# Performance work log

Hardware: AMD Instinct MI355X
Metric: run time of the kernel (lower is better)

Reference implementation:

```python
import jax, jax.numpy as jnp
import numpy as np

B, V, C, M, CM, D, OUT = 16, 16, 64, 32, 16, 128, 600
VOCAB = {"cond": 4000, "proc": 2000, "drug": 600, "lab_item": 700, "lab_value": 2000, "inj_item": 400, "inj_value": 2000}


def _gru(x, Wih, Whh, bih, bhh):
    """Batch-first torch-style GRU. x: [N,T,D] -> (outputs [N,T,D], h_T [N,D])."""
    Dh = Whh.shape[1]

    def step(h, xt):
        gi = xt @ Wih.T + bih
        gh = h @ Whh.T + bhh
        ir, iz, ig = jnp.split(gi, 3, axis=-1)
        hr, hz, hg = jnp.split(gh, 3, axis=-1)
        r = jax.nn.sigmoid(ir + hr)
        z = jax.nn.sigmoid(iz + hz)
        n = jnp.tanh(ig + r * hg)
        h = (1.0 - z) * n + z * h
        return h, h

    h0 = jnp.zeros((x.shape[0], Dh), x.dtype)
    hT, ys = jax.lax.scan(step, h0, jnp.swapaxes(x, 0, 1))
    return jnp.swapaxes(ys, 0, 1), hT


def _hetero_mp(feats, Wself, Wmsg):
    """Heterogeneous message passing over node types on the fully-connected
    monitor<->visit-feature bipartite pattern: each node type combines a self
    transform with a transformed mean of the other node types, then ReLU.
    feats: list of [N,D]; Wself/Wmsg: [T,D,D]."""
    stacked = jnp.stack(feats)  # [T,N,D]
    total = jnp.sum(stacked, axis=0)
    T = stacked.shape[0]
    outs = []
    for t in range(T):
        others = (total - stacked[t]) / (T - 1)
        outs.append(jax.nn.relu(stacked[t] @ Wself[t] + others @ Wmsg[t]))
    return outs


def _forward(codes_cond, codes_proc, codes_drug, codes_lab_item, codes_lab_value,
             codes_inj_item, codes_inj_value, weight, age,
             emb_cond, emb_proc, emb_drug, emb_lab_item, emb_lab_value,
             emb_inj_item, emb_inj_value,
             mgru_Wih, mgru_Whh, mgru_bih, mgru_bhh,
             vgru_Wih, vgru_Whh, vgru_bih, vgru_bhh,
             gnn_Wself, gnn_Wmsg,
             fc_weight_W, fc_weight_b, fc_age_W, fc_age_b,
             fc_patient_W, fc_patient_b):
    # ---- visit-event features: embedding lookup + sum-pool over codes ----
    vis = {}
    for k, codes, emb in (("cond", codes_cond, emb_cond),
                          ("proc", codes_proc, emb_proc),
                          ("drug", codes_drug, emb_drug)):
        vis[k] = jnp.sum(emb[codes], axis=2)  # [B,V,D]
    visit_keys = ("cond", "proc", "drug")

    # ---- monitor-event pairs: (item * value) embeddings, GNN, two-level GRU ----
    pairs = (
        (codes_lab_item, codes_lab_value, emb_lab_item, emb_lab_value, "lab_item", (0, 2, 3, 4)),
        (codes_inj_item, codes_inj_value, emb_inj_item, emb_inj_value, "inj_item", (1, 2, 3, 4)),
    )
    hid = {}
    for p, (ci, cv, ei, ev, ikey, gidx) in enumerate(pairs):
        mon = jnp.sum(ei[ci] * ev[cv], axis=3)  # [B,V,M,D]
        feats = [mon.reshape(-1, D)]  # monitor node type, [B*V*M, D]
        for k in visit_keys:  # visit features repeated across monitors
            feats.append(jnp.broadcast_to(vis[k][:, :, None, :], (B, V, M, D)).reshape(-1, D))
        outs = _hetero_mp(feats, gnn_Wself[p], gnn_Wmsg[p])
        for t, k in enumerate((ikey,) + visit_keys):
            g = gidx[t]
            # monitor-level GRU over the M monitors of each visit
            o, _ = _gru(outs[t].reshape(B * V, M, D), mgru_Wih[g], mgru_Whh[g], mgru_bih[g], mgru_bhh[g])
            last = o[:, -1, :].reshape(B, V, D)  # last monitor state per visit
            # visit-level GRU (source uses visit_gru[feature_key1] for all keys)
            _, h = _gru(last, vgru_Wih[p], vgru_Whh[p], vgru_bih[p], vgru_bhh[p])
            hid[k] = h if k not in hid else hid[k] + h

    # ---- weight / age scalar features ----
    for k, x, W, b, vi in (("weight", weight, fc_weight_W, fc_weight_b, 2),
                           ("age", age, fc_age_W, fc_age_b, 3)):
        mask = (x != 0.0)[..., None]  # [B,V,1]
        xe = (x[..., None] * W[:, 0] + b) * mask  # Linear(1->D) then zero-mask
        _, h = _gru(xe, vgru_Wih[vi], vgru_Whh[vi], vgru_bih[vi], vgru_bhh[vi])
        hid[k] = h

    # ---- concat in dict-insertion order, then ReLU + Linear head ----
    pe = jnp.concatenate([hid["lab_item"], hid["cond"], hid["proc"], hid["drug"],
                          hid["inj_item"], hid["weight"], hid["age"]], axis=-1)  # [B, 7D]
    return jax.nn.relu(pe) @ fc_patient_W.T + fc_patient_b  # [B, OUT]


def setup_inputs() -> dict:
    key = jax.random.key(0)
    ks = iter(jax.random.split(key, 64))

    def nrm(shape, s=0.1):
        return (jax.random.normal(next(ks), shape) * s).astype(jnp.float32)

    def emb_table(vsz):
        t = nrm((vsz, D), 1.0)
        return t.at[0].set(0.0)  # padding_idx=0 row is zero

    inp = {}
    inp["codes_cond"] = jax.random.randint(next(ks), (B, V, C), 0, VOCAB["cond"], dtype=jnp.int32)
    inp["codes_proc"] = jax.random.randint(next(ks), (B, V, C), 0, VOCAB["proc"], dtype=jnp.int32)
    inp["codes_drug"] = jax.random.randint(next(ks), (B, V, C), 0, VOCAB["drug"], dtype=jnp.int32)
    inp["codes_lab_item"] = jax.random.randint(next(ks), (B, V, M, CM), 0, VOCAB["lab_item"], dtype=jnp.int32)
    inp["codes_lab_value"] = jax.random.randint(next(ks), (B, V, M, CM), 0, VOCAB["lab_value"], dtype=jnp.int32)
    inp["codes_inj_item"] = jax.random.randint(next(ks), (B, V, M, CM), 0, VOCAB["inj_item"], dtype=jnp.int32)
    inp["codes_inj_value"] = jax.random.randint(next(ks), (B, V, M, CM), 0, VOCAB["inj_value"], dtype=jnp.int32)
    inp["weight"] = jax.random.uniform(next(ks), (B, V), minval=0.1, maxval=1.0, dtype=jnp.float32)
    inp["age"] = jax.random.uniform(next(ks), (B, V), minval=0.1, maxval=1.0, dtype=jnp.float32)
    inp["emb_cond"] = emb_table(VOCAB["cond"])
    inp["emb_proc"] = emb_table(VOCAB["proc"])
    inp["emb_drug"] = emb_table(VOCAB["drug"])
    inp["emb_lab_item"] = emb_table(VOCAB["lab_item"])
    inp["emb_lab_value"] = emb_table(VOCAB["lab_value"])
    inp["emb_inj_item"] = emb_table(VOCAB["inj_item"])
    inp["emb_inj_value"] = emb_table(VOCAB["inj_value"])
    inp["mgru_Wih"] = nrm((5, 3 * D, D))
    inp["mgru_Whh"] = nrm((5, 3 * D, D))
    inp["mgru_bih"] = nrm((5, 3 * D))
    inp["mgru_bhh"] = nrm((5, 3 * D))
    inp["vgru_Wih"] = nrm((4, 3 * D, D))
    inp["vgru_Whh"] = nrm((4, 3 * D, D))
    inp["vgru_bih"] = nrm((4, 3 * D))
    inp["vgru_bhh"] = nrm((4, 3 * D))
    inp["gnn_Wself"] = nrm((2, 4, D, D))
    inp["gnn_Wmsg"] = nrm((2, 4, D, D))
    inp["fc_weight_W"] = nrm((D, 1))
    inp["fc_weight_b"] = nrm((D,))
    inp["fc_age_W"] = nrm((D, 1))
    inp["fc_age_b"] = nrm((D,))
    inp["fc_patient_W"] = nrm((OUT, 7 * D))
    inp["fc_patient_b"] = nrm((OUT,))
    return inp


def reference(codes_cond, codes_proc, codes_drug, codes_lab_item, codes_lab_value,
              codes_inj_item, codes_inj_value, weight, age,
              emb_cond, emb_proc, emb_drug, emb_lab_item, emb_lab_value,
              emb_inj_item, emb_inj_value,
              mgru_Wih, mgru_Whh, mgru_bih, mgru_bhh,
              vgru_Wih, vgru_Whh, vgru_bih, vgru_bhh,
              gnn_Wself, gnn_Wmsg,
              fc_weight_W, fc_weight_b, fc_age_W, fc_age_b,
              fc_patient_W, fc_patient_b):
    return _forward(codes_cond, codes_proc, codes_drug, codes_lab_item, codes_lab_value,
                    codes_inj_item, codes_inj_value, weight, age,
                    emb_cond, emb_proc, emb_drug, emb_lab_item, emb_lab_value,
                    emb_inj_item, emb_inj_value,
                    mgru_Wih, mgru_Whh, mgru_bih, mgru_bhh,
                    vgru_Wih, vgru_Whh, vgru_bih, vgru_bhh,
                    gnn_Wself, gnn_Wmsg,
                    fc_weight_W, fc_weight_b, fc_age_W, fc_age_b,
                    fc_patient_W, fc_patient_b)
```

## Files before the change

kernel.cpp:

```cpp
#include <hip/hip_runtime.h>
#include <math.h>

#define B_   16
#define V_   16
#define C_   64
#define M_   32
#define CM_  16
#define D_   128
#define OUT_ 600
#define NSEQ 256
#define NROW 8192

typedef __attribute__((ext_vector_type(8))) short bf16x8;
typedef __attribute__((ext_vector_type(4))) short bf16x4;
typedef __attribute__((ext_vector_type(4))) float f32x4;

__device__ __forceinline__ unsigned short f2bf(float x) {
  union { float f; unsigned u; } v; v.f = x;
  unsigned r = v.u + 0x7fff + ((v.u >> 16) & 1);
  return (unsigned short)(r >> 16);
}
__device__ __forceinline__ float bf2f(short s) {
  union { unsigned u; float f; } v;
  v.u = ((unsigned)(unsigned short)s) << 16;
  return v.f;
}
__device__ __forceinline__ float fsig(float x)  { return __fdividef(1.f, 1.f + __expf(-x)); }
__device__ __forceinline__ float ftanh(float x) { return 1.f - 2.f*__fdividef(1.f, __expf(2.f*x) + 1.f); }

__device__ __forceinline__ void ldsbar() {
  asm volatile("s_waitcnt lgkmcnt(0)" ::: "memory");
  __builtin_amdgcn_s_barrier();
  asm volatile("" ::: "memory");
}

constexpr int OFF_VISB  = 98304;
constexpr int OFF_MONB  = 147456;
constexpr int OFF_W12T  = 2244608;
constexpr int OFF_WIHB  = 2375680;
constexpr int OFF_WIHTV = 2498560;
constexpr int OFF_XE    = 2695168;
constexpr int OFF_LAST  = 27926528;
constexpr int OFF_VH    = 29171712;

__global__ __launch_bounds__(256) void k_prepvis(
    const float* __restrict__ Wself, const float* __restrict__ Wmsg,
    const float* __restrict__ mWih,  const float* __restrict__ vWih,
    const float* __restrict__ wgt,   const float* __restrict__ age,
    const float* __restrict__ fwW,   const float* __restrict__ fwB,
    const float* __restrict__ faW,   const float* __restrict__ faB,
    const int* __restrict__ cc, const int* __restrict__ cp, const int* __restrict__ cd,
    const float* __restrict__ ec, const float* __restrict__ ep, const float* __restrict__ ed,
    const int* __restrict__ cli, const int* __restrict__ clv,
    const int* __restrict__ cii, const int* __restrict__ civ,
    const float* __restrict__ eli, const float* __restrict__ elv,
    const float* __restrict__ eii, const float* __restrict__ eiv,
    short* __restrict__ w12t, short* __restrict__ wihb,
    float* __restrict__ wihTv, float* __restrict__ xe,
    short* __restrict__ visb, short* __restrict__ monb)
{
  int bx = blockIdx.x, tid = threadIdx.x;
  if (bx < 1024) {
    int lin = bx*256 + tid;
    int pt = lin >> 15, rem = lin & 32767;
    int n = rem >> 8, k = rem & 255;
    float v;
    if (k < 128) v = Wself[pt*16384 + k*128 + n] - Wmsg[pt*16384 + k*128 + n]*(1.f/3.f);
    else         v = Wmsg[pt*16384 + (k-128)*128 + n]*(1.f/3.f);
    w12t[lin] = (short)f2bf(v);
  } else if (bx < 1984) {
    int lin = (bx-1024)*256 + tid;
    wihb[lin] = (short)f2bf(mWih[lin]);
  } else if (bx < 2752) {
    int lin = (bx-1984)*256 + tid;
    int g = lin / 49152, rem2 = lin % 49152;
    int k = rem2 / 384, j = rem2 % 384;
    wihTv[lin] = vWih[g*49152 + j*128 + k];
  } else if (bx < 3008) {
    int lin = (bx-2752)*256 + tid;
    int which = lin >> 15, rem2 = lin & 32767;
    int n = rem2 >> 7, d = rem2 & 127;
    float x  = which ? age[n] : wgt[n];
    float Wv = which ? faW[d] : fwW[d];
    float bb = which ? faB[d] : fwB[d];
    xe[lin] = (x != 0.0f) ? (x*Wv + bb) : 0.0f;
  } else if (bx < 3392) {
    int idx = (bx-3008)*256 + tid;
    int type = idx >> 15;
    int r = idx & 32767;
    int bv = r >> 7, d = r & 127;
    const int*   codes = (type==0) ? cc : (type==1) ? cp : cd;
    const float* emb   = (type==0) ? ec : (type==1) ? ep : ed;
    float acc = 0.f;
    for (int c = 0; c < C_; ++c) {
      int code = codes[bv*C_ + c];
      acc += emb[code*D_ + d];
    }
    visb[(type*NSEQ + bv)*D_ + d] = (short)f2bf(acc);
  } else {
    int rowid = (bx-3392)*2 + (tid >> 7);
    int p = rowid >> 13, bvm = rowid & 8191;
    int d = tid & 127;
    const int* ci = p ? cii : cli;  const int* cv = p ? civ : clv;
    const float* ei = p ? eii : eli; const float* ev = p ? eiv : elv;
    float acc = 0.f;
    #pragma unroll
    for (int c2 = 0; c2 < CM_; ++c2) {
      int iv = ci[bvm*CM_ + c2];
      int vv = cv[bvm*CM_ + c2];
      acc += ei[iv*D_ + d] * ev[vv*D_ + d];
    }
    monb[((size_t)p*NROW + bvm)*D_ + d] = (short)f2bf(acc);
  }
}

__global__ __launch_bounds__(512, 1) void k_ggru(
    const short* __restrict__ monb, const short* __restrict__ visb,
    const short* __restrict__ w12t, const short* __restrict__ wihb,
    const float* __restrict__ Wself, const float* __restrict__ mWhh,
    const float* __restrict__ mbih, const float* __restrict__ mbhh,
    float* __restrict__ last)
{
  const int run  = blockIdx.x >> 4;
  const int pair = blockIdx.x & 15;
  const int p = run >> 2, t = run & 3;
  const int g = (run % 4 == 0) ? (run / 4) : (run % 4 + 1);
  const int tid = threadIdx.x;
  const int w = tid >> 6;
  const int lane = tid & 63;
  const int c = lane & 15, q = lane >> 4;
  const int j = w*16 + c;

  __shared__ short hb[2][4][16][40];
  __shared__ __align__(16) short Ys[2][16][136];
  __shared__ __align__(16) short Xl[2][2048];

  for (int idx = tid; idx < 2*4*16*40; idx += 512)
    ((short*)hb)[idx] = 0;

  bf16x8 bW12[8];
  #pragma unroll
  for (int kt = 0; kt < 8; ++kt)
    bW12[kt] = *(const bf16x8*)(w12t + (size_t)run*32768 + (size_t)j*256 + kt*32 + q*8);

  bf16x8 bWs[4];
  if (t == 0) {
    const float* wsp = Wself + (size_t)run*16384 + j;
    #pragma unroll
    for (int kt = 0; kt < 4; ++kt) {
      bf16x8 tt;
      #pragma unroll
      for (int i = 0; i < 8; ++i)
        tt[i] = (short)f2bf(wsp[(kt*32 + q*8 + i)*128]);
      bWs[kt] = tt;
    }
  } else {
    #pragma unroll
    for (int kt = 0; kt < 4; ++kt) bWs[kt] = bW12[kt+4];
  }

  f32x4 Cpre = (f32x4){0.f,0.f,0.f,0.f};
  {
    const int bvc = pair*16 + c;
    #pragma unroll
    for (int kt = 0; kt < 4; ++kt) {
      const int ko = kt*32 + q*8;
      bf16x8 v0 = *(const bf16x8*)(visb + (size_t)(0*NSEQ + bvc)*128 + ko);
      bf16x8 v1 = *(const bf16x8*)(visb + (size_t)(1*NSEQ + bvc)*128 + ko);
      bf16x8 v2 = *(const bf16x8*)(visb + (size_t)(2*NSEQ + bvc)*128 + ko);
      bf16x8 vs;
      #pragma unroll
      for (int i = 0; i < 8; ++i)
        vs[i] = (short)f2bf(bf2f(v0[i]) + bf2f(v1[i]) + bf2f(v2[i]));
      Cpre = __builtin_amdgcn_mfma_f32_16x16x32_bf16(vs, bW12[kt+4], Cpre, 0, 0, 0);
    }
    if (t > 0) {
      #pragma unroll
      for (int kt = 0; kt < 4; ++kt) {
        const int ko = kt*32 + q*8;
        bf16x8 fv = *(const bf16x8*)(visb + (size_t)((t-1)*NSEQ + bvc)*128 + ko);
        Cpre = __builtin_amdgcn_mfma_f32_16x16x32_bf16(fv, bW12[kt], Cpre, 0, 0, 0);
      }
    }
  }

  bf16x8 bWih[3][4];
  #pragma unroll
  for (int gate = 0; gate < 3; ++gate)
    #pragma unroll
    for (int kt = 0; kt < 4; ++kt)
      bWih[gate][kt] = *(const bf16x8*)(wihb + ((size_t)g*384 + gate*128 + j)*128 + kt*32 + q*8);

  bf16x8 bWhh[3][4];
  #pragma unroll
  for (int gate = 0; gate < 3; ++gate) {
    const float* wp = mWhh + ((size_t)g*384 + gate*128 + j)*128 + q*8;
    #pragma unroll
    for (int kt = 0; kt < 4; ++kt) {
      float4 lo = *(const float4*)(wp + kt*32);
      float4 hi = *(const float4*)(wp + kt*32 + 4);
      bf16x8 tt;
      tt[0]=(short)f2bf(lo.x); tt[1]=(short)f2bf(lo.y); tt[2]=(short)f2bf(lo.z); tt[3]=(short)f2bf(lo.w);
      tt[4]=(short)f2bf(hi.x); tt[5]=(short)f2bf(hi.y); tt[6]=(short)f2bf(hi.z); tt[7]=(short)f2bf(hi.w);
      bWhh[gate][kt] = tt;
    }
  }
  const float bs0 = mbih[g*384 +       j] + mbhh[g*384 +       j];
  const float bs1 = mbih[g*384 + 128 + j] + mbhh[g*384 + 128 + j];
  const float bi2 = mbih[g*384 + 256 + j];
  const float bh2 = mbhh[g*384 + 256 + j];

  const bool stg = (tid < 256);
  const int xr_ = (tid >> 4) & 15, xu = tid & 15;
  const int bv = pair*16 + xr_;
  const short* fsrc = monb + ((size_t)p*NROW + (size_t)bv*32)*128 + xu*8;
  const int xdofs = xr_*128 + (((xu*16) ^ ((xr_&7)<<4)) >> 1);
  short* xdst0 = &Xl[0][xdofs];
  short* xdst1 = &Xl[1][xdofs];

  if (stg) {
    *(bf16x8*)xdst0 = *(const bf16x8*)fsrc;
    *(bf16x8*)xdst1 = *(const bf16x8*)(fsrc + 128);
  }
  float hf[4] = {0.f,0.f,0.f,0.f};
  const int ktw = w >> 1;
  const int kkw = (w & 1)*16 + c;
  ldsbar();

  {
    const char* xbase = (const char*)&Xl[0][0];
    f32x4 accY = Cpre;
    #pragma unroll
    for (int kt = 0; kt < 4; ++kt) {
      bf16x8 aX = *(const bf16x8*)(xbase + c*256 + ((kt*64 + q*16) ^ ((c&7)<<4)));
      accY = __builtin_amdgcn_mfma_f32_16x16x32_bf16(aX, bWs[kt], accY, 0, 0, 0);
    }
    #pragma unroll
    for (int reg = 0; reg < 4; ++reg)
      Ys[0][q*4 + reg][w*16 + c] = (short)f2bf(fmaxf(accY[reg], 0.f));
  }
  ldsbar();

  #pragma unroll 1
  for (int m = 0; m < 32; ++m) {
    const int cur = m & 1, nxt = cur ^ 1;

    bf16x8 xnext;
    if (stg && m < 30) xnext = *(const bf16x8*)(fsrc + (size_t)(m+2)*128);

    f32x4 accY = Cpre;
    if (m < 31) {
      const char* xbase = (const char*)&Xl[nxt][0];
      #pragma unroll
      for (int kt = 0; kt < 4; ++kt) {
        bf16x8 aX = *(const bf16x8*)(xbase + c*256 + ((kt*64 + q*16) ^ ((c&7)<<4)));
        accY = __builtin_amdgcn_mfma_f32_16x16x32_bf16(aX, bWs[kt], accY, 0, 0, 0);
      }
    }

    bf16x8 ah[4], a2[4];
    #pragma unroll
    for (int kt = 0; kt < 4; ++kt) {
      ah[kt] = *(const bf16x8*)&hb[cur][kt][c][q*8];
      a2[kt] = *(const bf16x8*)&Ys[cur][c][kt*32 + q*8];
    }
    f32x4 acc0 = (f32x4){0.f,0.f,0.f,0.f};
    f32x4 acc1 = (f32x4){0.f,0.f,0.f,0.f};
    f32x4 aG2  = (f32x4){0.f,0.f,0.f,0.f};
    f32x4 aH2  = (f32x4){0.f,0.f,0.f,0.f};
    #pragma unroll
    for (int kt = 0; kt < 4; ++kt) {
      acc0 = __builtin_amdgcn_mfma_f32_16x16x32_bf16(ah[kt], bWhh[0][kt], acc0, 0, 0, 0);
      acc1 = __builtin_amdgcn_mfma_f32_16x16x32_bf16(ah[kt], bWhh[1][kt], acc1, 0, 0, 0);
      aH2  = __builtin_amdgcn_mfma_f32_16x16x32_bf16(ah[kt], bWhh[2][kt], aH2,  0, 0, 0);
    }
    #pragma unroll
    for (int kt = 0; kt < 4; ++kt) {
      acc0 = __builtin_amdgcn_mfma_f32_16x16x32_bf16(a2[kt], bWih[0][kt], acc0, 0, 0, 0);
      acc1 = __builtin_amdgcn_mfma_f32_16x16x32_bf16(a2[kt], bWih[1][kt], acc1, 0, 0, 0);
      aG2  = __builtin_amdgcn_mfma_f32_16x16x32_bf16(a2[kt], bWih[2][kt], aG2,  0, 0, 0);
    }

    if (m < 31) {
      #pragma unroll
      for (int reg = 0; reg < 4; ++reg)
        Ys[nxt][q*4 + reg][w*16 + c] = (short)f2bf(fmaxf(accY[reg], 0.f));
    }
    if (stg && m < 30) *(bf16x8*)(cur ? xdst1 : xdst0) = xnext;

    #pragma unroll
    for (int reg = 0; reg < 4; ++reg) {
      float rr = fsig(acc0[reg] + bs0);
      float zz = fsig(acc1[reg] + bs1);
      float nn = ftanh(aG2[reg] + bi2 + rr*(aH2[reg] + bh2));
      float hnew = (1.f - zz)*nn + zz*hf[reg];
      hf[reg] = hnew;
      hb[nxt][ktw][q*4 + reg][kkw] = (short)f2bf(hnew);
    }
    ldsbar();
  }

  #pragma unroll
  for (int reg = 0; reg < 4; ++reg)
    last[((size_t)run*NSEQ + pair*16 + q*4 + reg)*D_ + j] = hf[reg];
}

__global__ __launch_bounds__(512, 1) void k_vgru(
    const float* __restrict__ last, const float* __restrict__ xe,
    const float* __restrict__ vWih, const float* __restrict__ vWhh,
    const float* __restrict__ vbih, const float* __restrict__ vbhh,
    float* __restrict__ vh)
{
  const int run = blockIdx.x;
  const int vidx = (run < 4) ? 0 : (run < 8) ? 1 : (run - 6);
  const int tid = threadIdx.x;
  const int w = tid >> 6;
  const int lane = tid & 63;
  const int c = lane & 15, q = lane >> 4;
  const int j = w*16 + c;

  __shared__ short hb[2][4][16][40];
  __shared__ __align__(16) short Xl[2][2048];

  for (int idx = tid; idx < 2*4*16*40; idx += 512)
    ((short*)hb)[idx] = 0;

  bf16x8 bWih[3][4], bWhh[3][4];
  #pragma unroll
  for (int gate = 0; gate < 3; ++gate) {
    const float* wi = vWih + ((size_t)vidx*384 + gate*128 + j)*128 + q*8;
    const float* wh = vWhh + ((size_t)vidx*384 + gate*128 + j)*128 + q*8;
    #pragma unroll
    for (int kt = 0; kt < 4; ++kt) {
      float4 a0 = *(const float4*)(wi + kt*32);
      float4 a1 = *(const float4*)(wi + kt*32 + 4);
      float4 b0 = *(const float4*)(wh + kt*32);
      float4 b1 = *(const float4*)(wh + kt*32 + 4);
      bf16x8 ti, th;
      ti[0]=(short)f2bf(a0.x); ti[1]=(short)f2bf(a0.y); ti[2]=(short)f2bf(a0.z); ti[3]=(short)f2bf(a0.w);
      ti[4]=(short)f2bf(a1.x); ti[5]=(short)f2bf(a1.y); ti[6]=(short)f2bf(a1.z); ti[7]=(short)f2bf(a1.w);
      th[0]=(short)f2bf(b0.x); th[1]=(short)f2bf(b0.y); th[2]=(short)f2bf(b0.z); th[3]=(short)f2bf(b0.w);
      th[4]=(short)f2bf(b1.x); th[5]=(short)f2bf(b1.y); th[6]=(short)f2bf(b1.z); th[7]=(short)f2bf(b1.w);
      bWih[gate][kt] = ti;
      bWhh[gate][kt] = th;
    }
  }
  const float bs0 = vbih[vidx*384 +       j] + vbhh[vidx*384 +       j];
  const float bs1 = vbih[vidx*384 + 128 + j] + vbhh[vidx*384 + 128 + j];
  const float bi2 = vbih[vidx*384 + 256 + j];
  const float bh2 = vbhh[vidx*384 + 256 + j];

  const bool stg = (tid < 256);
  const int xr_ = (tid >> 4) & 15, xu = tid & 15;
  const float* xsrc = ((run < 8) ? (last + ((size_t)run*NSEQ + xr_*16)*D_)
                                 : (xe + ((size_t)(run-8)*NSEQ + xr_*16)*D_)) + xu*8;
  const int xdofs = xr_*128 + (((xu*16) ^ ((xr_&7)<<4)) >> 1);
  short* xdst0 = &Xl[0][xdofs];
  short* xdst1 = &Xl[1][xdofs];

  auto stageX = [&](short* dst, int v) {
    const float* s = xsrc + (size_t)v*D_;
    float4 lo = *(const float4*)s;
    float4 hi = *(const float4*)(s + 4);
    bf16x8 t;
    t[0]=(short)f2bf(lo.x); t[1]=(short)f2bf(lo.y); t[2]=(short)f2bf(lo.z); t[3]=(short)f2bf(lo.w);
    t[4]=(short)f2bf(hi.x); t[5]=(short)f2bf(hi.y); t[6]=(short)f2bf(hi.z); t[7]=(short)f2bf(hi.w);
    *(bf16x8*)dst = t;
  };
  if (stg) { stageX(xdst0, 0); stageX(xdst1, 1); }

  float hf[4] = {0.f,0.f,0.f,0.f};
  const int ktw = w >> 1;
  const int kkw = (w & 1)*16 + c;
  ldsbar();

  f32x4 giA[3], giB[3];
  {
    const char* xbase = (const char*)&Xl[0][0];
    #pragma unroll
    for (int gate = 0; gate < 3; ++gate) giA[gate] = (f32x4){0.f,0.f,0.f,0.f};
    #pragma unroll
    for (int kt = 0; kt < 4; ++kt) {
      bf16x8 ax = *(const bf16x8*)(xbase + c*256 + ((kt*64 + q*16) ^ ((c&7)<<4)));
      giA[0] = __builtin_amdgcn_mfma_f32_16x16x32_bf16(ax, bWih[0][kt], giA[0], 0, 0, 0);
      giA[1] = __builtin_amdgcn_mfma_f32_16x16x32_bf16(ax, bWih[1][kt], giA[1], 0, 0, 0);
      giA[2] = __builtin_amdgcn_mfma_f32_16x16x32_bf16(ax, bWih[2][kt], giA[2], 0, 0, 0);
    }
  }
  ldsbar();

  auto step = [&](int v, f32x4 (&gcur)[3], f32x4 (&gnext)[3]) {
    const int cur = v & 1, nxt = cur ^ 1;
    if (v < 15) {
      const char* xbase = (const char*)&Xl[nxt][0];
      #pragma unroll
      for (int gate = 0; gate < 3; ++gate) gnext[gate] = (f32x4){0.f,0.f,0.f,0.f};
      #pragma unroll
      for (int kt = 0; kt < 4; ++kt) {
        bf16x8 ax = *(const bf16x8*)(xbase + c*256 + ((kt*64 + q*16) ^ ((c&7)<<4)));
        gnext[0] = __builtin_amdgcn_mfma_f32_16x16x32_bf16(ax, bWih[0][kt], gnext[0], 0, 0, 0);
        gnext[1] = __builtin_amdgcn_mfma_f32_16x16x32_bf16(ax, bWih[1][kt], gnext[1], 0, 0, 0);
        gnext[2] = __builtin_amdgcn_mfma_f32_16x16x32_bf16(ax, bWih[2][kt], gnext[2], 0, 0, 0);
      }
    }
    bf16x8 ah[4];
    #pragma unroll
    for (int kt = 0; kt < 4; ++kt)
      ah[kt] = *(const bf16x8*)&hb[cur][kt][c][q*8];
    f32x4 a0 = gcur[0], a1 = gcur[1];
    f32x4 aH2 = (f32x4){0.f,0.f,0.f,0.f};
    #pragma unroll
    for (int kt = 0; kt < 4; ++kt) {
      a0  = __builtin_amdgcn_mfma_f32_16x16x32_bf16(ah[kt], bWhh[0][kt], a0,  0, 0, 0);
      a1  = __builtin_amdgcn_mfma_f32_16x16x32_bf16(ah[kt], bWhh[1][kt], a1,  0, 0, 0);
      aH2 = __builtin_amdgcn_mfma_f32_16x16x32_bf16(ah[kt], bWhh[2][kt], aH2, 0, 0, 0);
    }
    if (stg && v < 14) stageX(cur ? xdst1 : xdst0, v + 2);
    #pragma unroll
    for (int reg = 0; reg < 4; ++reg) {
      float rr = fsig(a0[reg] + bs0);
      float zz = fsig(a1[reg] + bs1);
      float nn = ftanh(gcur[2][reg] + bi2 + rr*(aH2[reg] + bh2));
      float hnew = (1.f - zz)*nn + zz*hf[reg];
      hf[reg] = hnew;
      hb[nxt][ktw][q*4 + reg][kkw] = (short)f2bf(hnew);
    }
    ldsbar();
  };

  #pragma unroll 1
  for (int v2 = 0; v2 < 8; ++v2) {
    step(2*v2,     giA, giB);
    step(2*v2 + 1, giB, giA);
  }

  #pragma unroll
  for (int reg = 0; reg < 4; ++reg)
    vh[((size_t)run*16 + q*4 + reg)*D_ + j] = hf[reg];
}

__global__ __launch_bounds__(256) void k_head(
    const float* __restrict__ vh, const float* __restrict__ Wp,
    const float* __restrict__ bp, float* __restrict__ out)
{
  const int o = blockIdx.x;
  const int tid = threadIdx.x;
  const int b = tid & 15, kc = tid >> 4;
  const int a1[7] = {0,1,2,3,4,8,9};
  const int a2[7] = {-1,5,6,7,-1,-1,-1};
  const float4* wb = (const float4*)(Wp + (size_t)o*896 + kc*56);
  float acc = 0.f;
  #pragma unroll
  for (int i = 0; i < 14; ++i) {
// ... 53 lines not shown
  const float* Wself= (const float*)d_in[24];
  const float* Wmsg = (const float*)d_in[25];
  const float* fwW  = (const float*)d_in[26];
  const float* fwB  = (const float*)d_in[27];
  const float* faW  = (const float*)d_in[28];
  const float* faB  = (const float*)d_in[29];
  const float* Wp   = (const float*)d_in[30];
  const float* bp   = (const float*)d_in[31];
  float* out = (float*)d_out;
  float* ws  = (float*)d_ws;

  short* visb  = (short*)(ws + OFF_VISB);
  short* monb  = (short*)(ws + OFF_MONB);
  short* w12t  = (short*)(ws + OFF_W12T);
  short* wihb  = (short*)(ws + OFF_WIHB);
  float* wihTv = ws + OFF_WIHTV;
  float* xe    = ws + OFF_XE;
  float* last  = ws + OFF_LAST;
  float* vh    = ws + OFF_VH;

  k_prepvis<<<11584, 256, 0, stream>>>(Wself, Wmsg, mWih, vWih, wgt, age,
                                       fwW, fwB, faW, faB,
                                       cc, cp, cd, ec, ep, ed,
                                       cli, clv, cii, civ, eli, elv, eii, eiv,
                                       w12t, wihb, wihTv, xe, visb, monb);
  k_ggru<<<128, 512, 0, stream>>>(monb, visb, w12t, wihb, Wself,
                                  mWhh, mbih, mbhh, last);
  k_vgru<<<10, 512, 0, stream>>>(last, xe, vWih, vWhh, vbih, vbhh, vh);
  k_head<<<600, 256, 0, stream>>>(vh, Wp, bp, out);
}
```

Before: 245.9 us.

## Fuse visit GRU into monitor GRU kernel via last-block atomic counter handoff

Merges the separate visit-level GRU kernel into the monitor GRU kernel. Each of the 8 monitor runs uses an atomic counter so that the last of its 16 blocks goes on to run that run's visit GRU, and two extra blocks handle the weight/age sequences, which removes one kernel launch and its serialization gap. The visit GRU can start per run as soon as that run's monitor blocks finish, instead of waiting for all of them. It also drops the unused transposed vWih prep section from the prep kernel. The trade-off is threadfence/atomic overhead and a longer tail on the finishing blocks.

```diff
diff --git a/kernel.cpp b/kernel.cpp
--- a/kernel.cpp
+++ b/kernel.cpp
@@ -38,14 +38,14 @@
 constexpr int OFF_MONB  = 147456;
 constexpr int OFF_W12T  = 2244608;
 constexpr int OFF_WIHB  = 2375680;
-constexpr int OFF_WIHTV = 2498560;
+constexpr int OFF_CNT   = 2498560;
 constexpr int OFF_XE    = 2695168;
 constexpr int OFF_LAST  = 27926528;
 constexpr int OFF_VH    = 29171712;
 
 __global__ __launch_bounds__(256) void k_prepvis(
     const float* __restrict__ Wself, const float* __restrict__ Wmsg,
-    const float* __restrict__ mWih,  const float* __restrict__ vWih,
+    const float* __restrict__ mWih,
     const float* __restrict__ wgt,   const float* __restrict__ age,
     const float* __restrict__ fwW,   const float* __restrict__ fwB,
     const float* __restrict__ faW,   const float* __restrict__ faB,
@@ -56,11 +56,13 @@
     const float* __restrict__ eli, const float* __restrict__ elv,
     const float* __restrict__ eii, const float* __restrict__ eiv,
     short* __restrict__ w12t, short* __restrict__ wihb,
-    float* __restrict__ wihTv, float* __restrict__ xe,
-    short* __restrict__ visb, short* __restrict__ monb)
+    float* __restrict__ xe,
+    short* __restrict__ visb, short* __restrict__ monb,
+    int* __restrict__ cnt)
 {
   int bx = blockIdx.x, tid = threadIdx.x;
   if (bx < 1024) {
+    if (bx == 0 && tid < 16) cnt[tid] = 0;
     int lin = bx*256 + tid;
     int pt = lin >> 15, rem = lin & 32767;
     int n = rem >> 8, k = rem & 255;
@@ -71,21 +73,16 @@
   } else if (bx < 1984) {
     int lin = (bx-1024)*256 + tid;
     wihb[lin] = (short)f2bf(mWih[lin]);
-  } else if (bx < 2752) {
+  } else if (bx < 2240) {
     int lin = (bx-1984)*256 + tid;
-    int g = lin / 49152, rem2 = lin % 49152;
-    int k = rem2 / 384, j = rem2 % 384;
-    wihTv[lin] = vWih[g*49152 + j*128 + k];
-  } else if (bx < 3008) {
-    int lin = (bx-2752)*256 + tid;
     int which = lin >> 15, rem2 = lin & 32767;
     int n = rem2 >> 7, d = rem2 & 127;
     float x  = which ? age[n] : wgt[n];
     float Wv = which ? faW[d] : fwW[d];
     float bb = which ? faB[d] : fwB[d];
     xe[lin] = (x != 0.0f) ? (x*Wv + bb) : 0.0f;
-  } else if (bx < 3392) {
-    int idx = (bx-3008)*256 + tid;
+  } else if (bx < 2624) {
+    int idx = (bx-2240)*256 + tid;
     int type = idx >> 15;
     int r = idx & 32767;
     int bv = r >> 7, d = r & 127;
@@ -98,7 +95,7 @@
     }
     visb[(type*NSEQ + bv)*D_ + d] = (short)f2bf(acc);
   } else {
-    int rowid = (bx-3392)*2 + (tid >> 7);
+    int rowid = (bx-2624)*2 + (tid >> 7);
     int p = rowid >> 13, bvm = rowid & 8191;
     int d = tid & 127;
     const int* ci = p ? cii : cli;  const int* cv = p ? civ : clv;
@@ -119,12 +116,11 @@
     const short* __restrict__ w12t, const short* __restrict__ wihb,
     const float* __restrict__ Wself, const float* __restrict__ mWhh,
     const float* __restrict__ mbih, const float* __restrict__ mbhh,
-    float* __restrict__ last)
+    const float* __restrict__ vWih, const float* __restrict__ vWhh,
+    const float* __restrict__ vbih, const float* __restrict__ vbhh,
+    const float* __restrict__ xe, float* __restrict__ last,
+    float* __restrict__ vh, int* __restrict__ cnt)
 {
-  const int run  = blockIdx.x >> 4;
-  const int pair = blockIdx.x & 15;
-  const int p = run >> 2, t = run & 3;
-  const int g = (run % 4 == 0) ? (run / 4) : (run % 4 + 1);
   const int tid = threadIdx.x;
   const int w = tid >> 6;
   const int lane = tid & 63;
@@ -134,309 +130,316 @@
   __shared__ short hb[2][4][16][40];
   __shared__ __align__(16) short Ys[2][16][136];
   __shared__ __align__(16) short Xl[2][2048];
-
-  for (int idx = tid; idx < 2*4*16*40; idx += 512)
-    ((short*)hb)[idx] = 0;
-
-  bf16x8 bW12[8];
-  #pragma unroll
-  for (int kt = 0; kt < 8; ++kt)
-    bW12[kt] = *(const bf16x8*)(w12t + (size_t)run*32768 + (size_t)j*256 + kt*32 + q*8);
-
-  bf16x8 bWs[4];
-  if (t == 0) {
-    const float* wsp = Wself + (size_t)run*16384 + j;
-    #pragma unroll
-    for (int kt = 0; kt < 4; ++kt) {
-      bf16x8 tt;
-      #pragma unroll
-      for (int i = 0; i < 8; ++i)
-        tt[i] = (short)f2bf(wsp[(kt*32 + q*8 + i)*128]);
-      bWs[kt] = tt;
-    }
-  } else {
-    #pragma unroll
-    for (int kt = 0; kt < 4; ++kt) bWs[kt] = bW12[kt+4];
-  }
-
-  f32x4 Cpre = (f32x4){0.f,0.f,0.f,0.f};
-  {
-    const int bvc = pair*16 + c;
-    #pragma unroll
-    for (int kt = 0; kt < 4; ++kt) {
-      const int ko = kt*32 + q*8;
-      bf16x8 v0 = *(const bf16x8*)(visb + (size_t)(0*NSEQ + bvc)*128 + ko);
-      bf16x8 v1 = *(const bf16x8*)(visb + (size_t)(1*NSEQ + bvc)*128 + ko);
-      bf16x8 v2 = *(const bf16x8*)(visb + (size_t)(2*NSEQ + bvc)*128 + ko);
-      bf16x8 vs;
-      #pragma unroll
-      for (int i = 0; i < 8; ++i)
-        vs[i] = (short)f2bf(bf2f(v0[i]) + bf2f(v1[i]) + bf2f(v2[i]));
-      Cpre = __builtin_amdgcn_mfma_f32_16x16x32_bf16(vs, bW12[kt+4], Cpre, 0, 0, 0);
-    }
-    if (t > 0) {
+  __shared__ int dofin;
+
+  int vrun;
+
+  if (blockIdx.x < 128) {
+    const int run  = blockIdx.x >> 4;
+    const int pair = blockIdx.x & 15;
+    const int p = run >> 2, t = run & 3;
+    const int g = (run % 4 == 0) ? (run / 4) : (run % 4 + 1);
+
+    for (int idx = tid; idx < 2*4*16*40; idx += 512)
+      ((short*)hb)[idx] = 0;
+
+    bf16x8 bW12[8];
+    #pragma unroll
+    for (int kt = 0; kt < 8; ++kt)
+      bW12[kt] = *(const bf16x8*)(w12t + (size_t)run*32768 + (size_t)j*256 + kt*32 + q*8);
+
+    bf16x8 bWs[4];
+    if (t == 0) {
+      const float* wsp = Wself + (size_t)run*16384 + j;
+      #pragma unroll
+      for (int kt = 0; kt < 4; ++kt) {
+        bf16x8 tt;
+        #pragma unroll
+        for (int i = 0; i < 8; ++i)
+          tt[i] = (short)f2bf(wsp[(kt*32 + q*8 + i)*128]);
+        bWs[kt] = tt;
+      }
+    } else {
+      #pragma unroll
+      for (int kt = 0; kt < 4; ++kt) bWs[kt] = bW12[kt+4];
+    }
+
+    f32x4 Cpre = (f32x4){0.f,0.f,0.f,0.f};
+    {
+      const int bvc = pair*16 + c;
       #pragma unroll
       for (int kt = 0; kt < 4; ++kt) {
         const int ko = kt*32 + q*8;
-        bf16x8 fv = *(const bf16x8*)(visb + (size_t)((t-1)*NSEQ + bvc)*128 + ko);
-        Cpre = __builtin_amdgcn_mfma_f32_16x16x32_bf16(fv, bW12[kt], Cpre, 0, 0, 0);
-      }
-    }
-  }
-
-  bf16x8 bWih[3][4];
-  #pragma unroll
-  for (int gate = 0; gate < 3; ++gate)
-    #pragma unroll
-    for (int kt = 0; kt < 4; ++kt)
-      bWih[gate][kt] = *(const bf16x8*)(wihb + ((size_t)g*384 + gate*128 + j)*128 + kt*32 + q*8);
-
-  bf16x8 bWhh[3][4];
-  #pragma unroll
-  for (int gate = 0; gate < 3; ++gate) {
-    const float* wp = mWhh + ((size_t)g*384 + gate*128 + j)*128 + q*8;
-    #pragma unroll
-    for (int kt = 0; kt < 4; ++kt) {
-      float4 lo = *(const float4*)(wp + kt*32);
-      float4 hi = *(const float4*)(wp + kt*32 + 4);
-      bf16x8 tt;
-      tt[0]=(short)f2bf(lo.x); tt[1]=(short)f2bf(lo.y); tt[2]=(short)f2bf(lo.z); tt[3]=(short)f2bf(lo.w);
-      tt[4]=(short)f2bf(hi.x); tt[5]=(short)f2bf(hi.y); tt[6]=(short)f2bf(hi.z); tt[7]=(short)f2bf(hi.w);
-      bWhh[gate][kt] = tt;
-    }
-  }
-  const float bs0 = mbih[g*384 +       j] + mbhh[g*384 +       j];
-  const float bs1 = mbih[g*384 + 128 + j] + mbhh[g*384 + 128 + j];
-  const float bi2 = mbih[g*384 + 256 + j];
-  const float bh2 = mbhh[g*384 + 256 + j];
-
-  const bool stg = (tid < 256);
-  const int xr_ = (tid >> 4) & 15, xu = tid & 15;
-  const int bv = pair*16 + xr_;
-  const short* fsrc = monb + ((size_t)p*NROW + (size_t)bv*32)*128 + xu*8;
-  const int xdofs = xr_*128 + (((xu*16) ^ ((xr_&7)<<4)) >> 1);
-  short* xdst0 = &Xl[0][xdofs];
-  short* xdst1 = &Xl[1][xdofs];
-
-  if (stg) {
-    *(bf16x8*)xdst0 = *(const bf16x8*)fsrc;
-    *(bf16x8*)xdst1 = *(const bf16x8*)(fsrc + 128);
-  }
-  float hf[4] = {0.f,0.f,0.f,0.f};
-  const int ktw = w >> 1;
-  const int kkw = (w & 1)*16 + c;
-  ldsbar();
-
-  {
-    const char* xbase = (const char*)&Xl[0][0];
-    f32x4 accY = Cpre;
-    #pragma unroll
-    for (int kt = 0; kt < 4; ++kt) {
-      bf16x8 aX = *(const bf16x8*)(xbase + c*256 + ((kt*64 + q*16) ^ ((c&7)<<4)));
-      accY = __builtin_amdgcn_mfma_f32_16x16x32_bf16(aX, bWs[kt], accY, 0, 0, 0);
-    }
-    #pragma unroll
-    for (int reg = 0; reg < 4; ++reg)
-      Ys[0][q*4 + reg][w*16 + c] = (short)f2bf(fmaxf(accY[reg], 0.f));
-  }
-  ldsbar();
-
-  #pragma unroll 1
-  for (int m = 0; m < 32; ++m) {
-    const int cur = m & 1, nxt = cur ^ 1;
-
-    bf16x8 xnext;
-    if (stg && m < 30) xnext = *(const bf16x8*)(fsrc + (size_t)(m+2)*128);
-
-    f32x4 accY = Cpre;
-    if (m < 31) {
-      const char* xbase = (const char*)&Xl[nxt][0];
+        bf16x8 v0 = *(const bf16x8*)(visb + (size_t)(0*NSEQ + bvc)*128 + ko);
+        bf16x8 v1 = *(const bf16x8*)(visb + (size_t)(1*NSEQ + bvc)*128 + ko);
+        bf16x8 v2 = *(const bf16x8*)(visb + (size_t)(2*NSEQ + bvc)*128 + ko);
+        bf16x8 vs;
+        #pragma unroll
+        for (int i = 0; i < 8; ++i)
+          vs[i] = (short)f2bf(bf2f(v0[i]) + bf2f(v1[i]) + bf2f(v2[i]));
+        Cpre = __builtin_amdgcn_mfma_f32_16x16x32_bf16(vs, bW12[kt+4], Cpre, 0, 0, 0);
+      }
+      if (t > 0) {
+        #pragma unroll
+        for (int kt = 0; kt < 4; ++kt) {
+          const int ko = kt*32 + q*8;
+          bf16x8 fv = *(const bf16x8*)(visb + (size_t)((t-1)*NSEQ + bvc)*128 + ko);
+          Cpre = __builtin_amdgcn_mfma_f32_16x16x32_bf16(fv, bW12[kt], Cpre, 0, 0, 0);
+        }
+      }
+    }
+
+    bf16x8 bWih[3][4];
+    #pragma unroll
+    for (int gate = 0; gate < 3; ++gate)
+      #pragma unroll
+      for (int kt = 0; kt < 4; ++kt)
+        bWih[gate][kt] = *(const bf16x8*)(wihb + ((size_t)g*384 + gate*128 + j)*128 + kt*32 + q*8);
+
+    bf16x8 bWhh[3][4];
+    #pragma unroll
+    for (int gate = 0; gate < 3; ++gate) {
+      const float* wp = mWhh + ((size_t)g*384 + gate*128 + j)*128 + q*8;
+      #pragma unroll
+      for (int kt = 0; kt < 4; ++kt) {
+        float4 lo = *(const float4*)(wp + kt*32);
+        float4 hi = *(const float4*)(wp + kt*32 + 4);
+        bf16x8 tt;
+        tt[0]=(short)f2bf(lo.x); tt[1]=(short)f2bf(lo.y); tt[2]=(short)f2bf(lo.z); tt[3]=(short)f2bf(lo.w);
+        tt[4]=(short)f2bf(hi.x); tt[5]=(short)f2bf(hi.y); tt[6]=(short)f2bf(hi.z); tt[7]=(short)f2bf(hi.w);
+        bWhh[gate][kt] = tt;
+      }
+    }
+    const float bs0 = mbih[g*384 +       j] + mbhh[g*384 +       j];
+    const float bs1 = mbih[g*384 + 128 + j] + mbhh[g*384 + 128 + j];
+    const float bi2 = mbih[g*384 + 256 + j];
+    const float bh2 = mbhh[g*384 + 256 + j];
+
+    const bool stg = (tid < 256);
+    const int xr_ = (tid >> 4) & 15, xu = tid & 15;
+    const int bv = pair*16 + xr_;
+    const short* fsrc = monb + ((size_t)p*NROW + (size_t)bv*32)*128 + xu*8;
+    const int xdofs = xr_*128 + (((xu*16) ^ ((xr_&7)<<4)) >> 1);
+    short* xdst0 = &Xl[0][xdofs];
+    short* xdst1 = &Xl[1][xdofs];
+
+    if (stg) {
+      *(bf16x8*)xdst0 = *(const bf16x8*)fsrc;
+      *(bf16x8*)xdst1 = *(const bf16x8*)(fsrc + 128);
+    }
+    float hf[4] = {0.f,0.f,0.f,0.f};
+    const int ktw = w >> 1;
+    const int kkw = (w & 1)*16 + c;
+    ldsbar();
+
+    {
+      const char* xbase = (const char*)&Xl[0][0];
+      f32x4 accY = Cpre;
       #pragma unroll
       for (int kt = 0; kt < 4; ++kt) {
         bf16x8 aX = *(const bf16x8*)(xbase + c*256 + ((kt*64 + q*16) ^ ((c&7)<<4)));
         accY = __builtin_amdgcn_mfma_f32_16x16x32_bf16(aX, bWs[kt], accY, 0, 0, 0);
       }
-    }
-
-    bf16x8 ah[4], a2[4];
-    #pragma unroll
-    for (int kt = 0; kt < 4; ++kt) {
-      ah[kt] = *(const bf16x8*)&hb[cur][kt][c][q*8];
-      a2[kt] = *(const bf16x8*)&Ys[cur][c][kt*32 + q*8];
-    }
-    f32x4 acc0 = (f32x4){0.f,0.f,0.f,0.f};
-    f32x4 acc1 = (f32x4){0.f,0.f,0.f,0.f};
-    f32x4 aG2  = (f32x4){0.f,0.f,0.f,0.f};
-    f32x4 aH2  = (f32x4){0.f,0.f,0.f,0.f};
-    #pragma unroll
-    for (int kt = 0; kt < 4; ++kt) {
-      acc0 = __builtin_amdgcn_mfma_f32_16x16x32_bf16(ah[kt], bWhh[0][kt], acc0, 0, 0, 0);
-      acc1 = __builtin_amdgcn_mfma_f32_16x16x32_bf16(ah[kt], bWhh[1][kt], acc1, 0, 0, 0);
-      aH2  = __builtin_amdgcn_mfma_f32_16x16x32_bf16(ah[kt], bWhh[2][kt], aH2,  0, 0, 0);
-    }
-    #pragma unroll
-    for (int kt = 0; kt < 4; ++kt) {
-      acc0 = __builtin_amdgcn_mfma_f32_16x16x32_bf16(a2[kt], bWih[0][kt], acc0, 0, 0, 0);
-      acc1 = __builtin_amdgcn_mfma_f32_16x16x32_bf16(a2[kt], bWih[1][kt], acc1, 0, 0, 0);
-      aG2  = __builtin_amdgcn_mfma_f32_16x16x32_bf16(a2[kt], bWih[2][kt], aG2,  0, 0, 0);
-    }
-
-    if (m < 31) {
       #pragma unroll
       for (int reg = 0; reg < 4; ++reg)
-        Ys[nxt][q*4 + reg][w*16 + c] = (short)f2bf(fmaxf(accY[reg], 0.f));
-    }
-    if (stg && m < 30) *(bf16x8*)(cur ? xdst1 : xdst0) = xnext;
-
-    #pragma unroll
-    for (int reg = 0; reg < 4; ++reg) {
-      float rr = fsig(acc0[reg] + bs0);
-      float zz = fsig(acc1[reg] + bs1);
-      float nn = ftanh(aG2[reg] + bi2 + rr*(aH2[reg] + bh2));
-      float hnew = (1.f - zz)*nn + zz*hf[reg];
-      hf[reg] = hnew;
-      hb[nxt][ktw][q*4 + reg][kkw] = (short)f2bf(hnew);
+        Ys[0][q*4 + reg][w*16 + c] = (short)f2bf(fmaxf(accY[reg], 0.f));
     }
     ldsbar();
+
+    #pragma unroll 1
+    for (int m = 0; m < 32; ++m) {
+      const int cur = m & 1, nxt = cur ^ 1;
+      bf16x8 xnext;
+      if (stg && m < 30) xnext = *(const bf16x8*)(fsrc + (size_t)(m+2)*128);
+
+      f32x4 accY = Cpre;
+      if (m < 31) {
+        const char* xbase = (const char*)&Xl[nxt][0];
+        #pragma unroll
+        for (int kt = 0; kt < 4; ++kt) {
+          bf16x8 aX = *(const bf16x8*)(xbase + c*256 + ((kt*64 + q*16) ^ ((c&7)<<4)));
+          accY = __builtin_amdgcn_mfma_f32_16x16x32_bf16(aX, bWs[kt], accY, 0, 0, 0);
+        }
+      }
+
+      bf16x8 ah[4], a2[4];
+      #pragma unroll
+      for (int kt = 0; kt < 4; ++kt) {
+        ah[kt] = *(const bf16x8*)&hb[cur][kt][c][q*8];
+        a2[kt] = *(const bf16x8*)&Ys[cur][c][kt*32 + q*8];
+      }
+      f32x4 acc0 = (f32x4){0.f,0.f,0.f,0.f};
+      f32x4 acc1 = (f32x4){0.f,0.f,0.f,0.f};
+      f32x4 aG2  = (f32x4){0.f,0.f,0.f,0.f};
+      f32x4 aH2  = (f32x4){0.f,0.f,0.f,0.f};
+      #pragma unroll
+      for (int kt = 0; kt < 4; ++kt) {
+        acc0 = __builtin_amdgcn_mfma_f32_16x16x32_bf16(ah[kt], bWhh[0][kt], acc0, 0, 0, 0);
+        acc1 = __builtin_amdgcn_mfma_f32_16x16x32_bf16(ah[kt], bWhh[1][kt], acc1, 0, 0, 0);
+        aH2  = __builtin_amdgcn_mfma_f32_16x16x32_bf16(ah[kt], bWhh[2][kt], aH2,  0, 0, 0);
+      }
+      #pragma unroll
+      for (int kt = 0; kt < 4; ++kt) {
+        acc0 = __builtin_amdgcn_mfma_f32_16x16x32_bf16(a2[kt], bWih[0][kt], acc0, 0, 0, 0);
+        acc1 = __builtin_amdgcn_mfma_f32_16x16x32_bf16(a2[kt], bWih[1][kt], acc1, 0, 0, 0);
+        aG2  = __builtin_amdgcn_mfma_f32_16x16x32_bf16(a2[kt], bWih[2][kt], aG2,  0, 0, 0);
+      }
+
+      if (m < 31) {
+        #pragma unroll
+        for (int reg = 0; reg < 4; ++reg)
+          Ys[nxt][q*4 + reg][w*16 + c] = (short)f2bf(fmaxf(accY[reg], 0.f));
+      }
+      if (stg && m < 30) *(bf16x8*)(cur ? xdst1 : xdst0) = xnext;
+
+      #pragma unroll
+      for (int reg = 0; reg < 4; ++reg) {
+        float rr = fsig(acc0[reg] + bs0);
+        float zz = fsig(acc1[reg] + bs1);
+        float nn = ftanh(aG2[reg] + bi2 + rr*(aH2[reg] + bh2));
+        float hnew = (1.f - zz)*nn + zz*hf[reg];
+        hf[reg] = hnew;
+        hb[nxt][ktw][q*4 + reg][kkw] = (short)f2bf(hnew);
+      }
+      ldsbar();
+    }
+
+    #pragma unroll
+    for (int reg = 0; reg < 4; ++reg)
+      last[((size_t)run*NSEQ + pair*16 + q*4 + reg)*D_ + j] = hf[reg];
+
+    __threadfence();
+    if (tid == 0) {
+      int old = atomicAdd(&cnt[run], 1);
+      dofin = (old == 15) ? 1 : 0;
+    }
+    __syncthreads();
+    if (!dofin) return;
+    __threadfence();
+    vrun = run;
+  } else {
+    vrun = 8 + ((int)blockIdx.x - 128);
   }
 
-  #pragma unroll
-  for (int reg = 0; reg < 4; ++reg)
-    last[((size_t)run*NSEQ + pair*16 + q*4 + reg)*D_ + j] = hf[reg];
-}
-
-__global__ __launch_bounds__(512, 1) void k_vgru(
-    const float* __restrict__ last, const float* __restrict__ xe,
-    const float* __restrict__ vWih, const float* __restrict__ vWhh,
-    const float* __restrict__ vbih, const float* __restrict__ vbhh,
-    float* __restrict__ vh)
-{
-  const int run = blockIdx.x;
-  const int vidx = (run < 4) ? 0 : (run < 8) ? 1 : (run - 6);
-  const int tid = threadIdx.x;
-  const int w = tid >> 6;
-  const int lane = tid & 63;
-  const int c = lane & 15, q = lane >> 4;
-  const int j = w*16 + c;
-
-  __shared__ short hb[2][4][16][40];
-  __shared__ __align__(16) short Xl[2][2048];
-
-  for (int idx = tid; idx < 2*4*16*40; idx += 512)
-    ((short*)hb)[idx] = 0;
-
-  bf16x8 bWih[3][4], bWhh[3][4];
-  #pragma unroll
-  for (int gate = 0; gate < 3; ++gate) {
-    const float* wi = vWih + ((size_t)vidx*384 + gate*128 + j)*128 + q*8;
-    const float* wh = vWhh + ((size_t)vidx*384 + gate*128 + j)*128 + q*8;
-    #pragma unroll
-    for (int kt = 0; kt < 4; ++kt) {
-      float4 a0 = *(const float4*)(wi + kt*32);
-      float4 a1 = *(const float4*)(wi + kt*32 + 4);
-      float4 b0 = *(const float4*)(wh + kt*32);
-      float4 b1 = *(const float4*)(wh + kt*32 + 4);
-      bf16x8 ti, th;
-      ti[0]=(short)f2bf(a0.x); ti[1]=(short)f2bf(a0.y); ti[2]=(short)f2bf(a0.z); ti[3]=(short)f2bf(a0.w);
-      ti[4]=(short)f2bf(a1.x); ti[5]=(short)f2bf(a1.y); ti[6]=(short)f2bf(a1.z); ti[7]=(short)f2bf(a1.w);
-      th[0]=(short)f2bf(b0.x); th[1]=(short)f2bf(b0.y); th[2]=(short)f2bf(b0.z); th[3]=(short)f2bf(b0.w);
-      th[4]=(short)f2bf(b1.x); th[5]=(short)f2bf(b1.y); th[6]=(short)f2bf(b1.z); th[7]=(short)f2bf(b1.w);
-      bWih[gate][kt] = ti;
-      bWhh[gate][kt] = th;
-    }
+  {
+    const int vidx = (vrun < 4) ? 0 : (vrun < 8) ? 1 : (vrun - 6);
+
+    for (int idx = tid; idx < 2*4*16*40; idx += 512)
+      ((short*)hb)[idx] = 0;
+
+    bf16x8 vWihF[3][4], vWhhF[3][4];
+    #pragma unroll
+    for (int gate = 0; gate < 3; ++gate) {
+      const float* wi = vWih + ((size_t)vidx*384 + gate*128 + j)*128 + q*8;
+      const float* wh = vWhh + ((size_t)vidx*384 + gate*128 + j)*128 + q*8;
+      #pragma unroll
+      for (int kt = 0; kt < 4; ++kt) {
+        float4 a0 = *(const float4*)(wi + kt*32);
+        float4 a1 = *(const float4*)(wi + kt*32 + 4);
+        float4 b0 = *(const float4*)(wh + kt*32);
+        float4 b1 = *(const float4*)(wh + kt*32 + 4);
+        bf16x8 ti, th;
+        ti[0]=(short)f2bf(a0.x); ti[1]=(short)f2bf(a0.y); ti[2]=(short)f2bf(a0.z); ti[3]=(short)f2bf(a0.w);
+        ti[4]=(short)f2bf(a1.x); ti[5]=(short)f2bf(a1.y); ti[6]=(short)f2bf(a1.z); ti[7]=(short)f2bf(a1.w);
+        th[0]=(short)f2bf(b0.x); th[1]=(short)f2bf(b0.y); th[2]=(short)f2bf(b0.z); th[3]=(short)f2bf(b0.w);
+        th[4]=(short)f2bf(b1.x); th[5]=(short)f2bf(b1.y); th[6]=(short)f2bf(b1.z); th[7]=(short)f2bf(b1.w);
+        vWihF[gate][kt] = ti;
+        vWhhF[gate][kt] = th;
+      }
+    }
+    const float vs0 = vbih[vidx*384 +       j] + vbhh[vidx*384 +       j];
+    const float vs1 = vbih[vidx*384 + 128 + j] + vbhh[vidx*384 + 128 + j];
+    const float vi2 = vbih[vidx*384 + 256 + j];
+    const float vh2 = vbhh[vidx*384 + 256 + j];
+
+    const bool stg = (tid < 256);
+    const int xr_ = (tid >> 4) & 15, xu = tid & 15;
+    const float* xsrc = ((vrun < 8) ? (last + ((size_t)vrun*NSEQ + xr_*16)*D_)
+                                    : (xe + ((size_t)(vrun-8)*NSEQ + xr_*16)*D_)) + xu*8;
+    const int xdofs = xr_*128 + (((xu*16) ^ ((xr_&7)<<4)) >> 1);
+    short* xdst0 = &Xl[0][xdofs];
+    short* xdst1 = &Xl[1][xdofs];
+
+    auto stageX = [&](short* dst, int v) {
+      const float* s = xsrc + (size_t)v*D_;
+      float4 lo = *(const float4*)s;
+      float4 hi = *(const float4*)(s + 4);
+      bf16x8 t2;
+      t2[0]=(short)f2bf(lo.x); t2[1]=(short)f2bf(lo.y); t2[2]=(short)f2bf(lo.z); t2[3]=(short)f2bf(lo.w);
+      t2[4]=(short)f2bf(hi.x); t2[5]=(short)f2bf(hi.y); t2[6]=(short)f2bf(hi.z); t2[7]=(short)f2bf(hi.w);
+      *(bf16x8*)dst = t2;
+    };
+    if (stg) { stageX(xdst0, 0); stageX(xdst1, 1); }
+
+    float hf[4] = {0.f,0.f,0.f,0.f};
+    const int ktw = w >> 1;
+    const int kkw = (w & 1)*16 + c;
+    ldsbar();
+
+    f32x4 giA[3], giB[3];
+    {
+      const char* xbase = (const char*)&Xl[0][0];
+      #pragma unroll
+      for (int gate = 0; gate < 3; ++gate) giA[gate] = (f32x4){0.f,0.f,0.f,0.f};
+      #pragma unroll
+      for (int kt = 0; kt < 4; ++kt) {
+        bf16x8 ax = *(const bf16x8*)(xbase + c*256 + ((kt*64 + q*16) ^ ((c&7)<<4)));
+        giA[0] = __builtin_amdgcn_mfma_f32_16x16x32_bf16(ax, vWihF[0][kt], giA[0], 0, 0, 0);
+        giA[1] = __builtin_amdgcn_mfma_f32_16x16x32_bf16(ax, vWihF[1][kt], giA[1], 0, 0, 0);
+        giA[2] = __builtin_amdgcn_mfma_f32_16x16x32_bf16(ax, vWihF[2][kt], giA[2], 0, 0, 0);
+      }
+    }
+    ldsbar();
+
+    auto step = [&](int v, f32x4 (&gcur)[3], f32x4 (&gnext)[3]) {
+      const int cur = v & 1, nxt = cur ^ 1;
+      if (v < 15) {
+        const char* xbase = (const char*)&Xl[nxt][0];
+        #pragma unroll
+        for (int gate = 0; gate < 3; ++gate) gnext[gate] = (f32x4){0.f,0.f,0.f,0.f};
+        #pragma unroll
+        for (int kt = 0; kt < 4; ++kt) {
+          bf16x8 ax = *(const bf16x8*)(xbase + c*256 + ((kt*64 + q*16) ^ ((c&7)<<4)));
+          gnext[0] = __builtin_amdgcn_mfma_f32_16x16x32_bf16(ax, vWihF[0][kt], gnext[0], 0, 0, 0);
+          gnext[1] = __builtin_amdgcn_mfma_f32_16x16x32_bf16(ax, vWihF[1][kt], gnext[1], 0, 0, 0);
+          gnext[2] = __builtin_amdgcn_mfma_f32_16x16x32_bf16(ax, vWihF[2][kt], gnext[2], 0, 0, 0);
+        }
+      }
+      bf16x8 ah[4];
+      #pragma unroll
+      for (int kt = 0; kt < 4; ++kt)
+        ah[kt] = *(const bf16x8*)&hb[cur][kt][c][q*8];
+      f32x4 a0 = gcur[0], a1 = gcur[1];
+      f32x4 aH2 = (f32x4){0.f,0.f,0.f,0.f};
+      #pragma unroll
+      for (int kt = 0; kt < 4; ++kt) {
+        a0  = __builtin_amdgcn_mfma_f32_16x16x32_bf16(ah[kt], vWhhF[0][kt], a0,  0, 0, 0);
+        a1  = __builtin_amdgcn_mfma_f32_16x16x32_bf16(ah[kt], vWhhF[1][kt], a1,  0, 0, 0);
+        aH2 = __builtin_amdgcn_mfma_f32_16x16x32_bf16(ah[kt], vWhhF[2][kt], aH2, 0, 0, 0);
+      }
+      if (stg && v < 14) stageX(cur ? xdst1 : xdst0, v + 2);
+      #pragma unroll
+      for (int reg = 0; reg < 4; ++reg) {
+        float rr = fsig(a0[reg] + vs0);
+        float zz = fsig(a1[reg] + vs1);
+        float nn = ftanh(gcur[2][reg] + vi2 + rr*(aH2[reg] + vh2));
+        float hnew = (1.f - zz)*nn + zz*hf[reg];
+        hf[reg] = hnew;
+        hb[nxt][ktw][q*4 + reg][kkw] = (short)f2bf(hnew);
+      }
+      ldsbar();
+    };
+
+    #pragma unroll 1
+    for (int v2 = 0; v2 < 8; ++v2) {
+      step(2*v2,     giA, giB);
+      step(2*v2 + 1, giB, giA);
+    }
+
+    #pragma unroll
+    for (int reg = 0; reg < 4; ++reg)
+      vh[((size_t)vrun*16 + q*4 + reg)*D_ + j] = hf[reg];
   }
-  const float bs0 = vbih[vidx*384 +       j] + vbhh[vidx*384 +       j];
-  const float bs1 = vbih[vidx*384 + 128 + j] + vbhh[vidx*384 + 128 + j];
-  const float bi2 = vbih[vidx*384 + 256 + j];
-  const float bh2 = vbhh[vidx*384 + 256 + j];
-
-  const bool stg = (tid < 256);
-  const int xr_ = (tid >> 4) & 15, xu = tid & 15;
-  const float* xsrc = ((run < 8) ? (last + ((size_t)run*NSEQ + xr_*16)*D_)
-                                 : (xe + ((size_t)(run-8)*NSEQ + xr_*16)*D_)) + xu*8;
-  const int xdofs = xr_*128 + (((xu*16) ^ ((xr_&7)<<4)) >> 1);
-  short* xdst0 = &Xl[0][xdofs];
-  short* xdst1 = &Xl[1][xdofs];
-
-  auto stageX = [&](short* dst, int v) {
-    const float* s = xsrc + (size_t)v*D_;
-    float4 lo = *(const float4*)s;
-    float4 hi = *(const float4*)(s + 4);
-    bf16x8 t;
-    t[0]=(short)f2bf(lo.x); t[1]=(short)f2bf(lo.y); t[2]=(short)f2bf(lo.z); t[3]=(short)f2bf(lo.w);
-    t[4]=(short)f2bf(hi.x); t[5]=(short)f2bf(hi.y); t[6]=(short)f2bf(hi.z); t[7]=(short)f2bf(hi.w);
-    *(bf16x8*)dst = t;
-  };
-  if (stg) { stageX(xdst0, 0); stageX(xdst1, 1); }
-
-  float hf[4] = {0.f,0.f,0.f,0.f};
-  const int ktw = w >> 1;
-  const int kkw = (w & 1)*16 + c;
-  ldsbar();
-
-  f32x4 giA[3], giB[3];
-  {
-    const char* xbase = (const char*)&Xl[0][0];
-    #pragma unroll
-    for (int gate = 0; gate < 3; ++gate) giA[gate] = (f32x4){0.f,0.f,0.f,0.f};
-    #pragma unroll
-    for (int kt = 0; kt < 4; ++kt) {
-      bf16x8 ax = *(const bf16x8*)(xbase + c*256 + ((kt*64 + q*16) ^ ((c&7)<<4)));
-      giA[0] = __builtin_amdgcn_mfma_f32_16x16x32_bf16(ax, bWih[0][kt], giA[0], 0, 0, 0);
-      giA[1] = __builtin_amdgcn_mfma_f32_16x16x32_bf16(ax, bWih[1][kt], giA[1], 0, 0, 0);
-      giA[2] = __builtin_amdgcn_mfma_f32_16x16x32_bf16(ax, bWih[2][kt], giA[2], 0, 0, 0);
-    }
-  }
-  ldsbar();
-
-  auto step = [&](int v, f32x4 (&gcur)[3], f32x4 (&gnext)[3]) {
-    const int cur = v & 1, nxt = cur ^ 1;
-    if (v < 15) {
-      const char* xbase = (const char*)&Xl[nxt][0];
-      #pragma unroll
-      for (int gate = 0; gate < 3; ++gate) gnext[gate] = (f32x4){0.f,0.f,0.f,0.f};
-      #pragma unroll
-      for (int kt = 0; kt < 4; ++kt) {
-        bf16x8 ax = *(const bf16x8*)(xbase + c*256 + ((kt*64 + q*16) ^ ((c&7)<<4)));
-        gnext[0] = __builtin_amdgcn_mfma_f32_16x16x32_bf16(ax, bWih[0][kt], gnext[0], 0, 0, 0);
-        gnext[1] = __builtin_amdgcn_mfma_f32_16x16x32_bf16(ax, bWih[1][kt], gnext[1], 0, 0, 0);
-        gnext[2] = __builtin_amdgcn_mfma_f32_16x16x32_bf16(ax, bWih[2][kt], gnext[2], 0, 0, 0);
-      }
-    }
-    bf16x8 ah[4];
-    #pragma unroll
-    for (int kt = 0; kt < 4; ++kt)
-      ah[kt] = *(const bf16x8*)&hb[cur][kt][c][q*8];
-    f32x4 a0 = gcur[0], a1 = gcur[1];
-    f32x4 aH2 = (f32x4){0.f,0.f,0.f,0.f};
-    #pragma unroll
-    for (int kt = 0; kt < 4; ++kt) {
-      a0  = __builtin_amdgcn_mfma_f32_16x16x32_bf16(ah[kt], bWhh[0][kt], a0,  0, 0, 0);
-      a1  = __builtin_amdgcn_mfma_f32_16x16x32_bf16(ah[kt], bWhh[1][kt], a1,  0, 0, 0);
-      aH2 = __builtin_amdgcn_mfma_f32_16x16x32_bf16(ah[kt], bWhh[2][kt], aH2, 0, 0, 0);
-    }
-    if (stg && v < 14) stageX(cur ? xdst1 : xdst0, v + 2);
-    #pragma unroll
-    for (int reg = 0; reg < 4; ++reg) {
-      float rr = fsig(a0[reg] + bs0);
-      float zz = fsig(a1[reg] + bs1);
-      float nn = ftanh(gcur[2][reg] + bi2 + rr*(aH2[reg] + bh2));
-      float hnew = (1.f - zz)*nn + zz*hf[reg];
-      hf[reg] = hnew;
-      hb[nxt][ktw][q*4 + reg][kkw] = (short)f2bf(hnew);
-    }
-    ldsbar();
-  };
-
-  #pragma unroll 1
-  for (int v2 = 0; v2 < 8; ++v2) {
-    step(2*v2,     giA, giB);
-    step(2*v2 + 1, giB, giA);
-  }
-
-  #pragma unroll
-  for (int reg = 0; reg < 4; ++reg)
-    vh[((size_t)run*16 + q*4 + reg)*D_ + j] = hf[reg];
 }
 
 __global__ __launch_bounds__(256) void k_head(
@@ -520,18 +523,19 @@
   short* monb  = (short*)(ws + OFF_MONB);
   short* w12t  = (short*)(ws + OFF_W12T);
   short* wihb  = (short*)(ws + OFF_WIHB);
-  float* wihTv = ws + OFF_WIHTV;
+  int*   cnt   = (int*)  (ws + OFF_CNT);
   float* xe    = ws + OFF_XE;
   float* last  = ws + OFF_LAST;
   float* vh    = ws + OFF_VH;
 
-  k_prepvis<<<11584, 256, 0, stream>>>(Wself, Wmsg, mWih, vWih, wgt, age,
+  k_prepvis<<<10816, 256, 0, stream>>>(Wself, Wmsg, mWih, wgt, age,
                                        fwW, fwB, faW, faB,
                                        cc, cp, cd, ec, ep, ed,
                                        cli, clv, cii, civ, eli, elv, eii, eiv,
-                                       w12t, wihb, wihTv, xe, visb, monb);
-  k_ggru<<<128, 512, 0, stream>>>(monb, visb, w12t, wihb, Wself,
-                                  mWhh, mbih, mbhh, last);
-  k_vgru<<<10, 512, 0, stream>>>(last, xe, vWih, vWhh, vbih, vbhh, vh);
+                                       w12t, wihb, xe, visb, monb, cnt);
+  k_ggru<<<130, 512, 0, stream>>>(monb, visb, w12t, wihb, Wself,
+                                  mWhh, mbih, mbhh,
+                                  vWih, vWhh, vbih, vbhh,
+                                  xe, last, vh, cnt);
   k_head<<<600, 256, 0, stream>>>(vh, Wp, bp, out);
 }
```

New measurement: 273.4 us. +11.2%, slower.
